# Optimization experiments

Hardware: AMD Instinct MI355X
Metric: run time of the kernel (lower is better)

Reference implementation:

```python
import jax, jax.numpy as jnp
import numpy as np

B, H, W, C = 64, 56, 56, 192
HEADS = 6
WIN = (7, 7)
SHIFT = (3, 3)
N = WIN[0] * WIN[1]  # tokens per window = 49
EPS = 1e-5


def _rel_pos_index(ws):
    # standard Swin relative position index, shape (N, N), values in [0, (2wh-1)(2ww-1))
    coords = np.stack(np.meshgrid(np.arange(ws[0]), np.arange(ws[1]), indexing='ij'))
    cf = coords.reshape(2, -1)
    rel = (cf[:, :, None] - cf[:, None, :]).transpose(1, 2, 0)  # N,N,2
    rel[..., 0] += ws[0] - 1
    rel[..., 1] += ws[1] - 1
    rel[..., 0] *= 2 * ws[1] - 1
    return rel.sum(-1)


def _swin_attn_mask(h, w, ws, ss):
    # cyclic-shift attention mask, shape (nW, N, N), values {0, -100}
    img = np.zeros((h, w), dtype=np.float32)
    cnt = 0
    for hs in (slice(0, -ws[0]), slice(-ws[0], -ss[0]), slice(-ss[0], None)):
        for wsl in (slice(0, -ws[1]), slice(-ws[1], -ss[1]), slice(-ss[1], None)):
            img[hs, wsl] = cnt
            cnt += 1
    m = img.reshape(h // ws[0], ws[0], w // ws[1], ws[1]).transpose(0, 2, 1, 3).reshape(-1, N)
    am = m[:, None, :] - m[:, :, None]
    return np.where(am != 0, -100.0, 0.0).astype(np.float32)


def setup_inputs() -> dict:
    key = jax.random.key(0)
    ks = jax.random.split(key, 5)
    x = jax.random.normal(ks[0], (B, H, W, C), dtype=jnp.float32)
    mask_matrix = jnp.asarray(_swin_attn_mask(H, W, WIN, SHIFT))
    gamma = jnp.ones((C,), jnp.float32)
    beta = jnp.zeros((C,), jnp.float32)
    w_qkv = jax.random.normal(ks[1], (C, 3 * C), jnp.float32) * 0.02
    b_qkv = jnp.zeros((3 * C,), jnp.float32)
    rel_table = jax.random.normal(ks[2], ((2 * WIN[0] - 1) * (2 * WIN[1] - 1), HEADS), jnp.float32) * 0.02
    w_proj = jax.random.normal(ks[3], (C, C), jnp.float32) * 0.02
    b_proj = jnp.zeros((C,), jnp.float32)
    return {"x": x, "gamma": gamma, "beta": beta, "w_qkv": w_qkv, "b_qkv": b_qkv,
            "rel_table": rel_table, "w_proj": w_proj, "b_proj": b_proj,
            "mask_matrix": mask_matrix}


def reference(x, gamma, beta, w_qkv, b_qkv, rel_table, w_proj, b_proj, mask_matrix):
    b, h, w, c = x.shape
    hd = c // HEADS
    scale = hd ** -0.5

    # norm1 (LayerNorm over channels)
    mu = jnp.mean(x, axis=-1, keepdims=True)
    var = jnp.var(x, axis=-1, keepdims=True)
    x = (x - mu) * jax.lax.rsqrt(var + EPS) * gamma + beta

    # cyclic shift (H,W divisible by window -> no padding)
    sx = jnp.roll(x, shift=(-SHIFT[0], -SHIFT[1]), axis=(1, 2))

    # window partition -> (B*nW, N, C)
    nh, nw = h // WIN[0], w // WIN[1]
    win = sx.reshape(b, nh, WIN[0], nw, WIN[1], c).transpose(0, 1, 3, 2, 4, 5)
    win = win.reshape(-1, N, c)

    # window attention with relative position bias + shift mask
    qkv = (win @ w_qkv + b_qkv).reshape(-1, N, 3, HEADS, hd).transpose(2, 0, 3, 1, 4)
    q, k, v = qkv[0], qkv[1], qkv[2]  # (B_, heads, N, hd)
    attn = jnp.einsum('bhnd,bhmd->bhnm', q * scale, k)
    rpi = _rel_pos_index(WIN)
    bias = rel_table[rpi.reshape(-1)].reshape(N, N, HEADS).transpose(2, 0, 1)  # heads,N,N
    attn = attn + bias[None]
    nW = mask_matrix.shape[0]
    attn = attn.reshape(b, nW, HEADS, N, N) + mask_matrix[None, :, None]
    attn = jax.nn.softmax(attn.reshape(-1, HEADS, N, N), axis=-1)
    out = jnp.einsum('bhnm,bhmd->bhnd', attn, v).transpose(0, 2, 1, 3).reshape(-1, N, c)
    out = out @ w_proj + b_proj

    # window reverse -> (B,H,W,C)
    out = out.reshape(b, nh, nw, WIN[0], WIN[1], c).transpose(0, 1, 3, 2, 4, 5).reshape(b, h, w, c)

    # reverse cyclic shift
    return jnp.roll(out, shift=(SHIFT[0], SHIFT[1]), axis=(1, 2))
```

## Files before the change

kernel.cpp:

```cpp
#include <hip/hip_runtime.h>
#include <hip/hip_bf16.h>
#include <math.h>

typedef __bf16 bf16;
typedef __bf16 bf16x4 __attribute__((ext_vector_type(4)));
typedef __bf16 bf16x8 __attribute__((ext_vector_type(8)));
typedef float f32x4 __attribute__((ext_vector_type(4)));
typedef unsigned int u32x4 __attribute__((ext_vector_type(4)));

#define NHEADS 6
#define CDIM 192
#define IMG 56
#define NTOK 49
#define SHIFTV 3
#define XSTR 200
#define VSTR 72
#define SCALE 0.17677669529663687f

static __device__ __forceinline__ unsigned pack2bf(float lo, float hi) {
    unsigned short a = __builtin_bit_cast(unsigned short, (bf16)lo);
    unsigned short b = __builtin_bit_cast(unsigned short, (bf16)hi);
    return (unsigned)a | ((unsigned)b << 16);
}

__global__ void prep_weights(const float* __restrict__ w_qkv, const float* __restrict__ w_proj,
                             bf16* __restrict__ wqkvT, bf16* __restrict__ wprojT) {
    int i = blockIdx.x * 256 + threadIdx.x;
    if (i < 576 * 192) {
        int n = i / 192, k = i % 192;
        wqkvT[i] = (bf16)w_qkv[k * 576 + n];
    }
    if (i < 192 * 192) {
        int n = i / 192, k = i % 192;
        wprojT[i] = (bf16)w_proj[k * 192 + n];
    }
}

__global__ __launch_bounds__(512, 4) void swin_block(
    const float* __restrict__ x, const float* __restrict__ gamma, const float* __restrict__ beta,
    const bf16* __restrict__ wqkvT, const float* __restrict__ b_qkv,
    const float* __restrict__ rel_table, const bf16* __restrict__ wprojT,
    const float* __restrict__ b_proj, float* __restrict__ out)
{
    __shared__ __align__(16) bf16 BufA[64 * XSTR];
    __shared__ __align__(16) bf16 BufB[64 * XSTR];
    __shared__ __align__(16) bf16 VTs[CDIM * VSTR];
    __shared__ bf16 biasS[169 * NHEADS];

    const int blk  = blockIdx.x;
    const int bimg = blk >> 6;
    const int wy   = (blk >> 3) & 7;
    const int wx   = blk & 7;
    const int tid  = threadIdx.x;
    const int wave = tid >> 6;
    const int lane = tid & 63;

    for (int i = tid; i < 169 * NHEADS; i += 512) biasS[i] = (bf16)rel_table[i];

    {
        const float g0 = gamma[lane], g1 = gamma[lane + 64], g2 = gamma[lane + 128];
        const float b0 = beta[lane],  b1 = beta[lane + 64],  b2 = beta[lane + 128];
        for (int t = wave; t < 64; t += 8) {
            if (t < NTOK) {
                int ty = t / 7, tx = t % 7;
                int oy = (wy * 7 + ty + SHIFTV) % IMG;
                int ox = (wx * 7 + tx + SHIFTV) % IMG;
                const float* xp = x + (((size_t)bimg * IMG + oy) * IMG + ox) * CDIM;
                float v0 = xp[lane], v1 = xp[lane + 64], v2 = xp[lane + 128];
                float s = v0 + v1 + v2, ss = v0 * v0 + v1 * v1 + v2 * v2;
                #pragma unroll
                for (int off = 32; off; off >>= 1) { s += __shfl_xor(s, off); ss += __shfl_xor(ss, off); }
                float mu  = s * (1.f / 192.f);
                float var = ss * (1.f / 192.f) - mu * mu;
                float rs  = rsqrtf(var + 1e-5f);
                BufA[t * XSTR + lane      ] = (bf16)((v0 - mu) * rs * g0 + b0);
                BufA[t * XSTR + lane + 64 ] = (bf16)((v1 - mu) * rs * g1 + b1);
                BufA[t * XSTR + lane + 128] = (bf16)((v2 - mu) * rs * g2 + b2);
            } else {
                BufA[t * XSTR + lane      ] = (bf16)0.f;
                BufA[t * XSTR + lane + 64 ] = (bf16)0.f;
                BufA[t * XSTR + lane + 128] = (bf16)0.f;
            }
        }
    }
    __syncthreads();

    {
        const int lr = lane & 15, lq = lane >> 4;
        const int h0 = wave & 1;
        const int cg = wave >> 1;
        bf16x8 afrag[2][6];
        #pragma unroll
        for (int mm = 0; mm < 2; ++mm)
            #pragma unroll
            for (int k = 0; k < 6; ++k)
                afrag[mm][k] = *(const bf16x8*)&BufA[(32 * h0 + 16 * mm + lr) * XSTR + k * 32 + lq * 8];
        __syncthreads();

        for (int t = 0; t < 9; ++t) {
            const int nt = cg + 4 * t;
            const bf16* wp = wqkvT + (size_t)(nt * 16 + lr) * CDIM + lq * 8;
            bf16x8 bfrag[6];
            #pragma unroll
            for (int k = 0; k < 6; ++k) bfrag[k] = *(const bf16x8*)(wp + k * 32);
            f32x4 acc[2];
            acc[0] = f32x4{0.f, 0.f, 0.f, 0.f}; acc[1] = f32x4{0.f, 0.f, 0.f, 0.f};
            #pragma unroll
            for (int k = 0; k < 6; ++k)
                #pragma unroll
                for (int mm = 0; mm < 2; ++mm)
                    acc[mm] = __builtin_amdgcn_mfma_f32_16x16x32_bf16(afrag[mm][k], bfrag[k], acc[mm], 0, 0, 0);
            const int col  = nt * 16 + lr;
            const float bb = b_qkv[col];
            const int sect = col / CDIM;
            const int cc   = col % CDIM;
            if (sect == 2) {
                #pragma unroll
                for (int mm = 0; mm < 2; ++mm) {
                    bf16x4 v4;
                    #pragma unroll
                    for (int r = 0; r < 4; ++r) v4[r] = (bf16)(acc[mm][r] + bb);
                    *(bf16x4*)&VTs[cc * VSTR + 32 * h0 + 16 * mm + 4 * lq] = v4;
                }
            } else {
                bf16* dst = sect ? BufA : BufB;
                #pragma unroll
                for (int mm = 0; mm < 2; ++mm)
                    #pragma unroll
                    for (int r = 0; r < 4; ++r)
                        dst[(32 * h0 + 16 * mm + 4 * lq + r) * XSTR + cc] = (bf16)(acc[mm][r] + bb);
            }
        }
    }
    __syncthreads();

    {
        const int li = lane & 15, lq = lane >> 4;
        const int m  = wave & 3;
        const int hg = wave >> 2;
        const int i  = 16 * m + li;
        const int ic = i < NTOK ? i : NTOK - 1;
        const int iy = ic / 7, ix = ic % 7;
        const int ay = wy * 7 + iy, ax = wx * 7 + ix;
        const int ryi = (ay < 49) ? 0 : ((ay < 53) ? 1 : 2);
        const int rxi = (ax < 49) ? 0 : ((ax < 53) ? 1 : 2);
        int   rp[4][4];
        float msk[4][4];
        #pragma unroll
        for (int n = 0; n < 4; ++n)
            #pragma unroll
            for (int r = 0; r < 4; ++r) {
                int j = 16 * n + 4 * lq + r;
                if (j < NTOK) {
                    int jy = j / 7, jx = j % 7;
                    rp[n][r] = ((iy - jy + 6) * 13 + (ix - jx + 6)) * NHEADS;
                    int by = wy * 7 + jy, bx = wx * 7 + jx;
                    int ryj = (by < 49) ? 0 : ((by < 53) ? 1 : 2);
                    int rxj = (bx < 49) ? 0 : ((bx < 53) ? 1 : 2);
                    msk[n][r] = (ryi == ryj && rxi == rxj) ? 0.f : -100.f;
                } else { rp[n][r] = 0; msk[n][r] = -1e30f; }
            }
        const int src0 = li + 32 * (lq & 1);

        for (int hh = 0; hh < 3; ++hh) {
            const int h = hg * 3 + hh;
            bf16x8 bq = *(const bf16x8*)&BufB[(16 * m + li) * XSTR + h * 32 + lq * 8];
            f32x4 st[4];
            #pragma unroll
            for (int n = 0; n < 4; ++n) {
                bf16x8 ak = *(const bf16x8*)&BufA[(16 * n + li) * XSTR + h * 32 + lq * 8];
                st[n] = __builtin_amdgcn_mfma_f32_16x16x32_bf16(ak, bq, f32x4{0.f, 0.f, 0.f, 0.f}, 0, 0, 0);
            }
            float p[4][4];
            float vmax = -1e30f;
            #pragma unroll
            for (int n = 0; n < 4; ++n)
                #pragma unroll
                for (int r = 0; r < 4; ++r) {
                    float v = st[n][r] * SCALE + (float)biasS[rp[n][r] + h] + msk[n][r];
                    p[n][r] = v;
                    vmax = fmaxf(vmax, v);
                }
            vmax = fmaxf(vmax, __shfl_xor(vmax, 16));
            vmax = fmaxf(vmax, __shfl_xor(vmax, 32));
            float sum = 0.f;
            #pragma unroll
            for (int n = 0; n < 4; ++n)
                #pragma unroll
                for (int r = 0; r < 4; ++r) {
                    float e = __expf(p[n][r] - vmax);
                    p[n][r] = e; sum += e;
                }
            sum += __shfl_xor(sum, 16);
            sum += __shfl_xor(sum, 32);
            const float inv = 1.f / sum;
            unsigned pk[4][2];
            #pragma unroll
            for (int n = 0; n < 4; ++n)
                #pragma unroll
                for (int s = 0; s < 2; ++s)
                    pk[n][s] = pack2bf(p[n][2 * s] * inv, p[n][2 * s + 1] * inv);
            u32x4 ptw0, ptw1;
            #pragma unroll
            for (int w = 0; w < 4; ++w) {
                int srcl = src0 + 16 * (w >> 1);
                int s = w & 1;
                unsigned a0 = (unsigned)__shfl((int)pk[0][s], srcl);
                unsigned b0 = (unsigned)__shfl((int)pk[1][s], srcl);
                unsigned a1 = (unsigned)__shfl((int)pk[2][s], srcl);
                unsigned b1 = (unsigned)__shfl((int)pk[3][s], srcl);
                ptw0[w] = (lq & 2) ? b0 : a0;
                ptw1[w] = (lq & 2) ? b1 : a1;
            }
            bf16x8 bp0 = __builtin_bit_cast(bf16x8, ptw0);
            bf16x8 bp1 = __builtin_bit_cast(bf16x8, ptw1);
            f32x4 ot[2];
            #pragma unroll
            for (int dt = 0; dt < 2; ++dt) {
                const bf16* vrow = &VTs[(h * 32 + 16 * dt + li) * VSTR + lq * 8];
                bf16x8 av0 = *(const bf16x8*)(vrow);
                bf16x8 av1 = *(const bf16x8*)(vrow + 32);
                ot[dt] = __builtin_amdgcn_mfma_f32_16x16x32_bf16(av0, bp0, f32x4{0.f, 0.f, 0.f, 0.f}, 0, 0, 0);
                ot[dt] = __builtin_amdgcn_mfma_f32_16x16x32_bf16(av1, bp1, ot[dt], 0, 0, 0);
            }
            #pragma unroll
            for (int dt = 0; dt < 2; ++dt) {
                bf16x4 o4;
                #pragma unroll
                for (int r = 0; r < 4; ++r) o4[r] = (bf16)ot[dt][r];
                *(bf16x4*)&BufB[(16 * m + li) * XSTR + h * 32 + 16 * dt + 4 * lq] = o4;
            }
        }
    }
    __syncthreads();

    {
        const int lr = lane & 15, lq = lane >> 4;
        const int half = wave & 1;
        bf16x8 ofrag[2][6];
        #pragma unroll
        for (int mm = 0; mm < 2; ++mm)
            #pragma unroll
            for (int k = 0; k < 6; ++k)
                ofrag[mm][k] = *(const bf16x8*)&BufB[(16 * (2 * half + mm) + lr) * XSTR + k * 32 + lq * 8];
        for (int s3 = 0; s3 < 3; ++s3) {
            const int nt = (wave >> 1) + 4 * s3;
            const bf16* wp = wprojT + (size_t)(nt * 16 + lr) * CDIM + lq * 8;
            bf16x8 bfrag[6];
            #pragma unroll
            for (int k = 0; k < 6; ++k) bfrag[k] = *(const bf16x8*)(wp + k * 32);
            f32x4 acc[2];
            acc[0] = f32x4{0.f, 0.f, 0.f, 0.f}; acc[1] = f32x4{0.f, 0.f, 0.f, 0.f};
            #pragma unroll
            for (int k = 0; k < 6; ++k)
                #pragma unroll
                for (int mm = 0; mm < 2; ++mm)
                    acc[mm] = __builtin_amdgcn_mfma_f32_16x16x32_bf16(ofrag[mm][k], bfrag[k], acc[mm], 0, 0, 0);
            const int cc   = nt * 16 + lr;
            const float bb = b_proj[cc];
            #pragma unroll
            for (int mm = 0; mm < 2; ++mm)
                #pragma unroll
                for (int r = 0; r < 4; ++r) {
                    int row = 16 * (2 * half + mm) + lq * 4 + r;
                    if (row < NTOK) {
                        int ty = row / 7, tx = row % 7;
                        int oy = (wy * 7 + ty + SHIFTV) % IMG;
                        int ox = (wx * 7 + tx + SHIFTV) % IMG;
                        out[(((size_t)bimg * IMG + oy) * IMG + ox) * CDIM + cc] = acc[mm][r] + bb;
                    }
                }
        }
    }
}

extern "C" void kernel_launch(void* const* d_in, const int* in_sizes, int n_in,
                              void* d_out, int out_size, void* d_ws, size_t ws_size,
                              hipStream_t stream) {
    const float* x           = (const float*)d_in[0];
    const float* gamma       = (const float*)d_in[1];
    const float* beta        = (const float*)d_in[2];
    const float* w_qkv       = (const float*)d_in[3];
    const float* b_qkv       = (const float*)d_in[4];
    const float* rel_table   = (const float*)d_in[5];
    const float* w_proj      = (const float*)d_in[6];
    const float* b_proj      = (const float*)d_in[7];
    float* out = (float*)d_out;

    bf16* wqkvT  = (bf16*)d_ws;
    bf16* wprojT = (bf16*)((char*)d_ws + (size_t)576 * 192 * 2);

    prep_weights<<<432, 256, 0, stream>>>(w_qkv, w_proj, wqkvT, wprojT);
    swin_block<<<4096, 512, 0, stream>>>(x, gamma, beta, wqkvT, b_qkv, rel_table,
                                         wprojT, b_proj, out);
}
```

Measured before the change: 372.1 us.

## Precompute bias+mask table, swap MFMA operands for vectorized stores, retile projection

Builds a per-window-class combined relative-position bias and shift-mask table, scaled by log2(e), in the prep kernel. The attention loop can then use one fma plus exp2f instead of per-element index math, LDS bias gathers and mask adds. In the QKV and output projections the MFMA operands are swapped so each lane holds four consecutive columns. This allows bf16x4 LDS stores and f32x4 global stores with a per-row address computed once. The projection now gives each wave one 16-row tile and six column tiles, and modulo wraps become conditional subtracts. The cost is extra global reads of the bias table and a different register/work split in the projection.

```diff
diff --git a/kernel.cpp b/kernel.cpp
--- a/kernel.cpp
+++ b/kernel.cpp
@@ -15,6 +15,7 @@
 #define SHIFTV 3
 #define XSTR 200
 #define VSTR 72
+#define LOG2E 1.4426950408889634f
 #define SCALE 0.17677669529663687f
 
 static __device__ __forceinline__ unsigned pack2bf(float lo, float hi) {
@@ -24,7 +25,9 @@
 }
 
 __global__ void prep_weights(const float* __restrict__ w_qkv, const float* __restrict__ w_proj,
-                             bf16* __restrict__ wqkvT, bf16* __restrict__ wprojT) {
+                             const float* __restrict__ rel_table,
+                             bf16* __restrict__ wqkvT, bf16* __restrict__ wprojT,
+                             bf16* __restrict__ biasG) {
     int i = blockIdx.x * 256 + threadIdx.x;
     if (i < 576 * 192) {
         int n = i / 192, k = i % 192;
@@ -34,18 +37,30 @@
         int n = i / 192, k = i % 192;
         wprojT[i] = (bf16)w_proj[k * 192 + n];
     }
+    if (i < 24 * 64 * 64) {
+        int j = i & 63, ii = (i >> 6) & 63, t = i >> 12;
+        int h = t % 6, c = t / 6;
+        float val = -100.f;
+        if (ii < 49 && j < 49) {
+            int iy = ii / 7, ix = ii % 7, jy = j / 7, jx = j % 7;
+            int rp = (iy - jy + 6) * 13 + (ix - jx + 6);
+            bool ym = !(c & 2) || ((iy < 4) == (jy < 4));
+            bool xm = !(c & 1) || ((ix < 4) == (jx < 4));
+            val = rel_table[rp * 6 + h] + ((ym && xm) ? 0.f : -100.f);
+        }
+        biasG[i] = (bf16)(val * LOG2E);
+    }
 }
 
 __global__ __launch_bounds__(512, 4) void swin_block(
     const float* __restrict__ x, const float* __restrict__ gamma, const float* __restrict__ beta,
     const bf16* __restrict__ wqkvT, const float* __restrict__ b_qkv,
-    const float* __restrict__ rel_table, const bf16* __restrict__ wprojT,
+    const bf16* __restrict__ biasG, const bf16* __restrict__ wprojT,
     const float* __restrict__ b_proj, float* __restrict__ out)
 {
     __shared__ __align__(16) bf16 BufA[64 * XSTR];
     __shared__ __align__(16) bf16 BufB[64 * XSTR];
     __shared__ __align__(16) bf16 VTs[CDIM * VSTR];
-    __shared__ bf16 biasS[169 * NHEADS];
 
     const int blk  = blockIdx.x;
     const int bimg = blk >> 6;
@@ -55,16 +70,14 @@
     const int wave = tid >> 6;
     const int lane = tid & 63;
 
-    for (int i = tid; i < 169 * NHEADS; i += 512) biasS[i] = (bf16)rel_table[i];
-
     {
         const float g0 = gamma[lane], g1 = gamma[lane + 64], g2 = gamma[lane + 128];
         const float b0 = beta[lane],  b1 = beta[lane + 64],  b2 = beta[lane + 128];
         for (int t = wave; t < 64; t += 8) {
             if (t < NTOK) {
                 int ty = t / 7, tx = t % 7;
-                int oy = (wy * 7 + ty + SHIFTV) % IMG;
-                int ox = (wx * 7 + tx + SHIFTV) % IMG;
+                int oy = wy * 7 + ty + SHIFTV; if (oy >= IMG) oy -= IMG;
+                int ox = wx * 7 + tx + SHIFTV; if (ox >= IMG) ox -= IMG;
                 const float* xp = x + (((size_t)bimg * IMG + oy) * IMG + ox) * CDIM;
                 float v0 = xp[lane], v1 = xp[lane + 64], v2 = xp[lane + 128];
                 float s = v0 + v1 + v2, ss = v0 * v0 + v1 * v1 + v2 * v2;
@@ -103,18 +116,17 @@
             bf16x8 bfrag[6];
             #pragma unroll
             for (int k = 0; k < 6; ++k) bfrag[k] = *(const bf16x8*)(wp + k * 32);
+            const int sect = nt / 12;
             f32x4 acc[2];
             acc[0] = f32x4{0.f, 0.f, 0.f, 0.f}; acc[1] = f32x4{0.f, 0.f, 0.f, 0.f};
-            #pragma unroll
-            for (int k = 0; k < 6; ++k)
-                #pragma unroll
-                for (int mm = 0; mm < 2; ++mm)
-                    acc[mm] = __builtin_amdgcn_mfma_f32_16x16x32_bf16(afrag[mm][k], bfrag[k], acc[mm], 0, 0, 0);
-            const int col  = nt * 16 + lr;
-            const float bb = b_qkv[col];
-            const int sect = col / CDIM;
-            const int cc   = col % CDIM;
             if (sect == 2) {
+                #pragma unroll
+                for (int k = 0; k < 6; ++k)
+                    #pragma unroll
+                    for (int mm = 0; mm < 2; ++mm)
+                        acc[mm] = __builtin_amdgcn_mfma_f32_16x16x32_bf16(afrag[mm][k], bfrag[k], acc[mm], 0, 0, 0);
+                const int cc   = (nt - 24) * 16 + lr;
+                const float bb = b_qkv[384 + cc];
                 #pragma unroll
                 for (int mm = 0; mm < 2; ++mm) {
                     bf16x4 v4;
@@ -123,12 +135,22 @@
                     *(bf16x4*)&VTs[cc * VSTR + 32 * h0 + 16 * mm + 4 * lq] = v4;
                 }
             } else {
+                #pragma unroll
+                for (int k = 0; k < 6; ++k)
+                    #pragma unroll
+                    for (int mm = 0; mm < 2; ++mm)
+                        acc[mm] = __builtin_amdgcn_mfma_f32_16x16x32_bf16(bfrag[k], afrag[mm][k], acc[mm], 0, 0, 0);
+                const int col0 = nt * 16 + 4 * lq;
+                const f32x4 bq4 = *(const f32x4*)&b_qkv[col0];
+                const int ccl  = (nt % 12) * 16 + 4 * lq;
                 bf16* dst = sect ? BufA : BufB;
                 #pragma unroll
-                for (int mm = 0; mm < 2; ++mm)
+                for (int mm = 0; mm < 2; ++mm) {
+                    bf16x4 v4;
                     #pragma unroll
-                    for (int r = 0; r < 4; ++r)
-                        dst[(32 * h0 + 16 * mm + 4 * lq + r) * XSTR + cc] = (bf16)(acc[mm][r] + bb);
+                    for (int r = 0; r < 4; ++r) v4[r] = (bf16)(acc[mm][r] + bq4[r]);
+                    *(bf16x4*)&dst[(32 * h0 + 16 * mm + lr) * XSTR + ccl] = v4;
+                }
             }
         }
     }
@@ -138,30 +160,12 @@
         const int li = lane & 15, lq = lane >> 4;
         const int m  = wave & 3;
         const int hg = wave >> 2;
-        const int i  = 16 * m + li;
-        const int ic = i < NTOK ? i : NTOK - 1;
-        const int iy = ic / 7, ix = ic % 7;
-        const int ay = wy * 7 + iy, ax = wx * 7 + ix;
-        const int ryi = (ay < 49) ? 0 : ((ay < 53) ? 1 : 2);
-        const int rxi = (ax < 49) ? 0 : ((ax < 53) ? 1 : 2);
-        int   rp[4][4];
-        float msk[4][4];
+        const int cls = ((wy == 7) ? 2 : 0) | ((wx == 7) ? 1 : 0);
+        const bf16* bgp = biasG + (((size_t)cls * 6 + hg * 3) * 64 + (16 * m + li)) * 64 + 4 * lq;
+        const int src0 = li + 32 * (lq & 1);
+        const float SC = SCALE * LOG2E;
+
         #pragma unroll
-        for (int n = 0; n < 4; ++n)
-            #pragma unroll
-            for (int r = 0; r < 4; ++r) {
-                int j = 16 * n + 4 * lq + r;
-                if (j < NTOK) {
-                    int jy = j / 7, jx = j % 7;
-                    rp[n][r] = ((iy - jy + 6) * 13 + (ix - jx + 6)) * NHEADS;
-                    int by = wy * 7 + jy, bx = wx * 7 + jx;
-                    int ryj = (by < 49) ? 0 : ((by < 53) ? 1 : 2);
-                    int rxj = (bx < 49) ? 0 : ((bx < 53) ? 1 : 2);
-                    msk[n][r] = (ryi == ryj && rxi == rxj) ? 0.f : -100.f;
-                } else { rp[n][r] = 0; msk[n][r] = -1e30f; }
-            }
-        const int src0 = li + 32 * (lq & 1);
-
         for (int hh = 0; hh < 3; ++hh) {
             const int h = hg * 3 + hh;
             bf16x8 bq = *(const bf16x8*)&BufB[(16 * m + li) * XSTR + h * 32 + lq * 8];
@@ -171,24 +175,27 @@
                 bf16x8 ak = *(const bf16x8*)&BufA[(16 * n + li) * XSTR + h * 32 + lq * 8];
                 st[n] = __builtin_amdgcn_mfma_f32_16x16x32_bf16(ak, bq, f32x4{0.f, 0.f, 0.f, 0.f}, 0, 0, 0);
             }
+            bf16x4 b4[4];
+            #pragma unroll
+            for (int n = 0; n < 4; ++n) b4[n] = *(const bf16x4*)(bgp + hh * 4096 + 16 * n);
             float p[4][4];
-            float vmax = -1e30f;
+            float umax = -1e30f;
             #pragma unroll
             for (int n = 0; n < 4; ++n)
                 #pragma unroll
                 for (int r = 0; r < 4; ++r) {
-                    float v = st[n][r] * SCALE + (float)biasS[rp[n][r] + h] + msk[n][r];
+                    float v = fmaf(st[n][r], SC, (float)b4[n][r]);
                     p[n][r] = v;
-                    vmax = fmaxf(vmax, v);
+                    umax = fmaxf(umax, v);
                 }
-            vmax = fmaxf(vmax, __shfl_xor(vmax, 16));
-            vmax = fmaxf(vmax, __shfl_xor(vmax, 32));
+            umax = fmaxf(umax, __shfl_xor(umax, 16));
+            umax = fmaxf(umax, __shfl_xor(umax, 32));
             float sum = 0.f;
             #pragma unroll
             for (int n = 0; n < 4; ++n)
                 #pragma unroll
                 for (int r = 0; r < 4; ++r) {
-                    float e = __expf(p[n][r] - vmax);
+                    float e = exp2f(p[n][r] - umax);
                     p[n][r] = e; sum += e;
                 }
             sum += __shfl_xor(sum, 16);
@@ -235,41 +242,38 @@
     __syncthreads();
 
     {
-        const int lr = lane & 15, lq = lane >> 4;
-        const int half = wave & 1;
-        bf16x8 ofrag[2][6];
+        const int li = lane & 15, lq = lane >> 4;
+        const int tg  = wave & 3;
+        const int ch2 = wave >> 2;
+        bf16x8 ofrag[6];
         #pragma unroll
-        for (int mm = 0; mm < 2; ++mm)
+        for (int k = 0; k < 6; ++k)
+            ofrag[k] = *(const bf16x8*)&BufB[(16 * tg + li) * XSTR + k * 32 + lq * 8];
+        const int row = 16 * tg + li;
+        const bool valid = row < NTOK;
+        int ty = row / 7, tx = row % 7;
+        int oy = wy * 7 + ty + SHIFTV; if (oy >= IMG) oy -= IMG;
+        int ox = wx * 7 + tx + SHIFTV; if (ox >= IMG) ox -= IMG;
+        float* orow = out + (((size_t)bimg * IMG + oy) * IMG + ox) * CDIM;
+
+        for (int s3 = 0; s3 < 6; ++s3) {
+            const int nt = ch2 * 6 + s3;
+            const bf16* wp = wprojT + (size_t)(nt * 16 + li) * CDIM + lq * 8;
+            bf16x8 wfrag[6];
+            #pragma unroll
+            for (int k = 0; k < 6; ++k) wfrag[k] = *(const bf16x8*)(wp + k * 32);
+            f32x4 acc = f32x4{0.f, 0.f, 0.f, 0.f};
             #pragma unroll
             for (int k = 0; k < 6; ++k)
-                ofrag[mm][k] = *(const bf16x8*)&BufB[(16 * (2 * half + mm) + lr) * XSTR + k * 32 + lq * 8];
-        for (int s3 = 0; s3 < 3; ++s3) {
-            const int nt = (wave >> 1) + 4 * s3;
-            const bf16* wp = wprojT + (size_t)(nt * 16 + lr) * CDIM + lq * 8;
-            bf16x8 bfrag[6];
-            #pragma unroll
-            for (int k = 0; k < 6; ++k) bfrag[k] = *(const bf16x8*)(wp + k * 32);
-            f32x4 acc[2];
-            acc[0] = f32x4{0.f, 0.f, 0.f, 0.f}; acc[1] = f32x4{0.f, 0.f, 0.f, 0.f};
-            #pragma unroll
-            for (int k = 0; k < 6; ++k)
-                #pragma unroll
-                for (int mm = 0; mm < 2; ++mm)
-                    acc[mm] = __builtin_amdgcn_mfma_f32_16x16x32_bf16(ofrag[mm][k], bfrag[k], acc[mm], 0, 0, 0);
-            const int cc   = nt * 16 + lr;
-            const float bb = b_proj[cc];
-            #pragma unroll
-            for (int mm = 0; mm < 2; ++mm)
-                #pragma unroll
-                for (int r = 0; r < 4; ++r) {
-                    int row = 16 * (2 * half + mm) + lq * 4 + r;
-                    if (row < NTOK) {
-                        int ty = row / 7, tx = row % 7;
-                        int oy = (wy * 7 + ty + SHIFTV) % IMG;
-                        int ox = (wx * 7 + tx + SHIFTV) % IMG;
-                        out[(((size_t)bimg * IMG + oy) * IMG + ox) * CDIM + cc] = acc[mm][r] + bb;
-                    }
-                }
+                acc = __builtin_amdgcn_mfma_f32_16x16x32_bf16(wfrag[k], ofrag[k], acc, 0, 0, 0);
+            const int c0 = nt * 16 + 4 * lq;
+            const f32x4 bp = *(const f32x4*)&b_proj[c0];
+            if (valid) {
+                f32x4 v;
+                #pragma unroll
+                for (int r = 0; r < 4; ++r) v[r] = acc[r] + bp[r];
+                *(f32x4*)&orow[c0] = v;
+            }
         }
     }
 }
@@ -288,9 +292,10 @@
     float* out = (float*)d_out;
 
     bf16* wqkvT  = (bf16*)d_ws;
-    bf16* wprojT = (bf16*)((char*)d_ws + (size_t)576 * 192 * 2);
-
-    prep_weights<<<432, 256, 0, stream>>>(w_qkv, w_proj, wqkvT, wprojT);
-    swin_block<<<4096, 512, 0, stream>>>(x, gamma, beta, wqkvT, b_qkv, rel_table,
+    bf16* wprojT = (bf16*)((char*)d_ws + 221184);
+    bf16* biasG  = (bf16*)((char*)d_ws + 221184 + 73728);
+
+    prep_weights<<<432, 256, 0, stream>>>(w_qkv, w_proj, rel_table, wqkvT, wprojT, biasG);
+    swin_block<<<4096, 512, 0, stream>>>(x, gamma, beta, wqkvT, b_qkv, biasG,
                                          wprojT, b_proj, out);
 }
```

Result: slower. 430.7 us (+15.8%).
